# Kernel optimization log

Measured on AMD Instinct MI355X. Metric: run time of the kernel, lower is better.

## Reference

```python
import jax, jax.numpy as jnp
import numpy as np

P = 2          # SamplesLoss p=2
BLUR = 0.05    # eps_final = BLUR**P = 0.0025
SCALING = 0.8  # annealing factor per iteration (on the blur scale)


def _cost(x, y):
    # geomloss cost for p=2: |x - y|^2 / 2, shape (N, M)
    x2 = jnp.sum(x * x, axis=-1)
    y2 = jnp.sum(y * y, axis=-1)
    return 0.5 * (x2[:, None] + y2[None, :] - 2.0 * (x @ y.T))


def _softmin(eps, C, h):
    # -eps * log sum_j exp(h_j - C_ij / eps); h already contains log-weights
    return -eps * jax.nn.logsumexp(h[None, :] - C / eps, axis=1)


def _eps_schedule(x, y):
    # geomloss scaling_parameters / epsilon_schedule with diameter from bounding box
    xn, yn = np.asarray(x), np.asarray(y)
    mins = np.minimum(xn.min(0), yn.min(0))
    maxs = np.maximum(xn.max(0), yn.max(0))
    diameter = float(np.linalg.norm(maxs - mins))
    eps_list = ([diameter ** P]
                + [float(np.exp(e)) for e in np.arange(P * np.log(diameter), P * np.log(BLUR), P * np.log(SCALING))]
                + [BLUR ** P])
    return eps_list


def _sinkhorn_divergence(x, y, eps_list):
    # Debiased Sinkhorn divergence S_eps(x, y), geomloss sinkhorn_tensorized
    N, M = x.shape[0], y.shape[0]
    sg = jax.lax.stop_gradient
    C_xy, C_yx = _cost(x, y), _cost(y, x)
    C_xx, C_yy = _cost(x, sg(x)), _cost(y, sg(y))  # geomloss detaches 2nd arg
    # The annealing loop runs with autograd disabled in geomloss:
    Cxy_, Cyx_, Cxx_, Cyy_ = sg(C_xy), sg(C_yx), sg(C_xx), sg(C_yy)
    a_log = jnp.full((N,), -np.log(N), dtype=x.dtype)  # log uniform weights
    b_log = jnp.full((M,), -np.log(M), dtype=y.dtype)
    e0 = eps_list[0]
    f_aa = _softmin(e0, Cxx_, a_log)
    g_bb = _softmin(e0, Cyy_, b_log)
    g_ab = _softmin(e0, Cyx_, a_log)
    f_ba = _softmin(e0, Cxy_, b_log)
    for eps in eps_list:  # fixed schedule, not a data-dim loop
        ft_ba = _softmin(eps, Cxy_, b_log + g_ab / eps)
        gt_ab = _softmin(eps, Cyx_, a_log + f_ba / eps)
        ft_aa = _softmin(eps, Cxx_, a_log + f_aa / eps)
        gt_bb = _softmin(eps, Cyy_, b_log + g_bb / eps)
        f_ba, g_ab = 0.5 * (f_ba + ft_ba), 0.5 * (g_ab + gt_ab)
        f_aa, g_bb = 0.5 * (f_aa + ft_aa), 0.5 * (g_bb + gt_bb)
    # Final extrapolation step (the only one geomloss differentiates through):
    eps = eps_list[-1]
    f_ba, g_ab = (_softmin(eps, C_xy, sg(b_log + g_ab / eps)),
                  _softmin(eps, C_yx, sg(a_log + f_ba / eps)))
    f_aa = _softmin(eps, C_xx, sg(a_log + f_aa / eps))
    g_bb = _softmin(eps, C_yy, sg(b_log + g_bb / eps))
    # scal with uniform weights == mean
    return jnp.mean(f_ba - f_aa) + jnp.mean(g_ab - g_bb)


def setup_inputs() -> dict:
    key = jax.random.key(0)
    kx, kt = jax.random.split(key)
    x = jax.random.normal(kx, (4096, 64), dtype=jnp.float32)
    target = jax.random.normal(kt, (4096, 64), dtype=jnp.float32)
    return {"x": x, "target": target}


def reference(x, target):
    eps_list = _eps_schedule(x, target)  # concrete schedule from data diameter
    return _sinkhorn_divergence(x, target, eps_list)
```

## Files before the change

### kernel.cpp

```cpp
#include <hip/hip_runtime.h>
#include <math.h>

#define NPTS 4096
#define DIM  64
#define MAX_ITERS 37

#define ALOG (-8.317766166719343f)
#define L2E  (1.4426950408889634f)
#define LN2  (0.6931471805599453f)

#if __has_builtin(__builtin_amdgcn_exp2f)
#define EXP2F(x) __builtin_amdgcn_exp2f(x)
#else
#define EXP2F(x) exp2f(x)
#endif
#if __has_builtin(__builtin_amdgcn_logf)
#define LOG2F(x) __builtin_amdgcn_logf(x)
#else
#define LOG2F(x) log2f(x)
#endif

typedef _Float16 f16x8 __attribute__((ext_vector_type(8)));
typedef float    f32x4 __attribute__((ext_vector_type(4)));

__device__ __forceinline__ void multi_barrier(int* st, int idx, int nsub,
                                              int* lsense) {
    __syncthreads();
    if (threadIdx.x == 0) {
        int s = *lsense ^ 1;
        __threadfence();
        int sub = idx >> 5;
        int prev = __hip_atomic_fetch_add(st + sub * 16, 1, __ATOMIC_ACQ_REL,
                                          __HIP_MEMORY_SCOPE_AGENT);
        if (prev == 31) {
            int pm = __hip_atomic_fetch_add(st + 512, 1, __ATOMIC_ACQ_REL,
                                            __HIP_MEMORY_SCOPE_AGENT);
            if (pm == nsub - 1) {
                for (int i = 0; i < nsub; i++)
                    __hip_atomic_store(st + i * 16, 0, __ATOMIC_RELAXED,
                                       __HIP_MEMORY_SCOPE_AGENT);
                __hip_atomic_store(st + 512, 0, __ATOMIC_RELAXED,
                                   __HIP_MEMORY_SCOPE_AGENT);
                __hip_atomic_store(st + 544, s, __ATOMIC_RELEASE,
                                   __HIP_MEMORY_SCOPE_AGENT);
            } else {
                while (__hip_atomic_load(st + 544, __ATOMIC_ACQUIRE,
                                         __HIP_MEMORY_SCOPE_AGENT) != s)
                    __builtin_amdgcn_s_sleep(8);
            }
        } else {
            while (__hip_atomic_load(st + 544, __ATOMIC_ACQUIRE,
                                     __HIP_MEMORY_SCOPE_AGENT) != s)
                __builtin_amdgcn_s_sleep(8);
        }
        *lsense = s;
        __threadfence();
    }
    __syncthreads();
}

__device__ __forceinline__ void multi_barrier_g(int* st, int idx, int nsub,
                                                int* lsense) {
    __syncthreads();
    if (threadIdx.x == 0) {
        int s = *lsense ^ 1;
        __threadfence();
        int sub = idx >> 5;
        int prev = __hip_atomic_fetch_add(st + sub * 16, 1, __ATOMIC_ACQ_REL,
                                          __HIP_MEMORY_SCOPE_AGENT);
        if (prev == 31) {
            int pm = __hip_atomic_fetch_add(st + 1536, 1, __ATOMIC_ACQ_REL,
                                            __HIP_MEMORY_SCOPE_AGENT);
            if (pm == nsub - 1) {
                for (int i = 0; i < nsub; i++)
                    __hip_atomic_store(st + i * 16, 0, __ATOMIC_RELAXED,
                                       __HIP_MEMORY_SCOPE_AGENT);
                __hip_atomic_store(st + 1536, 0, __ATOMIC_RELAXED,
                                   __HIP_MEMORY_SCOPE_AGENT);
                __hip_atomic_store(st + 1600, s, __ATOMIC_RELEASE,
                                   __HIP_MEMORY_SCOPE_AGENT);
            } else {
                while (__hip_atomic_load(st + 1600, __ATOMIC_ACQUIRE,
                                         __HIP_MEMORY_SCOPE_AGENT) != s)
                    __builtin_amdgcn_s_sleep(8);
            }
        } else {
            while (__hip_atomic_load(st + 1600, __ATOMIC_ACQUIRE,
                                     __HIP_MEMORY_SCOPE_AGENT) != s)
                __builtin_amdgcn_s_sleep(8);
        }
        *lsense = s;
        __threadfence();
    }
    __syncthreads();
}

__global__ __launch_bounds__(256, 8) void mega8_kernel(
        const float* __restrict__ x, const float* __restrict__ y,
        _Float16* __restrict__ X16, _Float16* __restrict__ Y16,
        float* __restrict__ x2, float* __restrict__ y2,
        float* __restrict__ pmn, float* __restrict__ pmx,
        int* hdr, float* __restrict__ sched,
        float* __restrict__ F, float* __restrict__ H, float* __restrict__ P,
        int* bar, float* __restrict__ out)
{
    const int b  = blockIdx.x;
    const int tt = threadIdx.x;
    int senseG = 0, senseL = 0;

    int* stL = bar + (b >> 10) * 2048;
    int* stG = bar + 2 * 2048;
    const int idxL = b & 1023;

    __shared__ float hs[256];
    __shared__ _Float16 Bs[2][64][72];

    {
        int g = b * 256 + tt;
        if (g < NPTS * DIM) {
            float xv = x[g], yv = y[g];
            X16[g] = (_Float16)xv;
            Y16[g] = (_Float16)yv;
            float sx = xv * xv, sy = yv * yv;
            for (int o = 32; o > 0; o >>= 1) {
                sx += __shfl_xor(sx, o, 64);
                sy += __shfl_xor(sy, o, 64);
            }
            if ((tt & 63) == 0) { x2[g >> 6] = sx; y2[g >> 6] = sy; }
        }
        if (b < 128) {
            float mn = INFINITY, mx = -INFINITY;
            for (int gg = b * 256 + tt; gg < NPTS * DIM; gg += 128 * 256) {
                float v = x[gg]; mn = fminf(mn, v); mx = fmaxf(mx, v);
                float w = y[gg]; mn = fminf(mn, w); mx = fmaxf(mx, w);
            }
            float* smn = hs;
            float* smx = (float*)&Bs[0][0][0];
            smn[tt] = mn; smx[tt] = mx;
            __syncthreads();
            if (tt < 64) {
                for (int qq = 1; qq < 4; qq++) {
                    mn = fminf(mn, smn[tt + 64 * qq]);
                    mx = fmaxf(mx, smx[tt + 64 * qq]);
                }
                pmn[b * 64 + tt] = mn;
                pmx[b * 64 + tt] = mx;
            }
        }
    }
    multi_barrier_g(stG, b, 64, &senseG);

    if (b == 0) {
        float* r2 = hs;
        if (tt < 64) {
            float mn = INFINITY, mx = -INFINITY;
            for (int bb = 0; bb < 128; bb++) {
                mn = fminf(mn, pmn[bb * 64 + tt]);
                mx = fmaxf(mx, pmx[bb * 64 + tt]);
            }
            float range = mx - mn;
            r2[tt] = range * range;
        }
        __syncthreads();
        if (tt == 0) {
            float ss = 0.f;
            for (int k = 0; k < 64; k++) ss += r2[k];
            float diam_f = sqrtf(ss);
            double diam = (double)diam_f;
            double start = 2.0 * log(diam);
            double stop  = 2.0 * log(0.05);
            double step  = 2.0 * log(0.8);
            int n_ar = (int)ceil((stop - start) / step);
            if (n_ar < 0) n_ar = 0;
            int ne = n_ar + 2;
            if (ne > 63) ne = 63;
            sched[0] = (float)(diam * diam);
            for (int k = 0; k < n_ar && (1 + k) < 63; k++)
                sched[1 + k] = (float)exp(start + step * (double)k);
            sched[ne - 1] = 0.0025f;
            for (int k = ne; k < 64; k++) sched[k] = 0.0025f;
            hdr[0] = ne;
        }
    }
    multi_barrier_g(stG, b, 64, &senseG);

    const int n_eps = *(volatile int*)hdr;

    const int mat = b >> 9, rb = (b >> 4) & 31, cs = b & 15;
    const _Float16* Am = (mat == 0 || mat == 2) ? X16 : Y16;
    const _Float16* Bm = (mat == 1 || mat == 2) ? X16 : Y16;
    const int matc = (mat < 2) ? (1 - mat) : mat;
    const float* sqc = (matc == 0 || matc == 2) ? x2 : y2;
    const int c0 = cs * 256, r0 = rb * 128;
    const int wv = tt >> 6, lane = tt & 63, q = lane >> 4, lo = lane & 15;
    const int srow = tt >> 2, scol = (tt & 3) * 16;

    f16x8 a[2][2];
#pragma unroll
    for (int rt = 0; rt < 2; rt++) {
        const _Float16* ar = Am + (size_t)(r0 + wv * 32 + rt * 16 + lo) * DIM + q * 8;
        a[rt][0] = *(const f16x8*)ar;
        a[rt][1] = *(const f16x8*)(ar + 32);
    }
    const _Float16* Bsrc0 = Bm + (size_t)(c0 + srow) * DIM + scol;

    for (int p = 0; p <= n_eps + 2; p++) {
        const int t = (p == 0) ? -2 : (p == n_eps + 2) ? -1 : (p - 1);
        const bool do_main = (t < 0) || (t < n_eps);

        f16x8 t0a, t0b;
        if (do_main) {
            t0a = *(const f16x8*)Bsrc0;
            t0b = *(const f16x8*)(Bsrc0 + 8);
        }

        if (t == -2) {
            float inv2i = L2E / sched[0];
            hs[tt] = ALOG * L2E - 0.5f * sqc[c0 + tt] * inv2i;
        } else if (t == -1) {
            hs[tt] = H[mat * 4096 + c0 + tt];
        } else {
            int pp = (t == 0) ? 1 : ((t - 1) & 1);
            const float* Pm = P + pp * 524288;
            const float* Ps = Pm + 262144;
            float epsp = sched[(t == 0) ? 0 : (t - 1)];
            float inv2c = L2E / sched[t];
            int row = c0 + tt;
            int base = (matc * 16) * NPTS + row;
            float M = -INFINITY;
#pragma unroll
            for (int qq = 0; qq < 16; qq++) M = fmaxf(M, Pm[base + qq * NPTS]);
            float S = 0.f;
#pragma unroll
            for (int qq = 0; qq < 16; qq++)
                S += Ps[base + qq * NPTS] * EXP2F(Pm[base + qq * NPTS] - M);
            float sq = sqc[row];
            float res = 0.5f * sq - epsp * LN2 * (M + LOG2F(S));
            float fnew = (t == 0) ? res
                       : 0.5f * (F[((t - 1) & 1) * 16384 + matc * 4096 + row] + res);
            float h = ALOG * L2E + (fnew - 0.5f * sq) * inv2c;
            hs[tt] = h;
            if (rb == 0) {
                F[(t & 1) * 16384 + matc * 4096 + row] = fnew;
                H[mat * 4096 + row] = h;
            }
        }

        if (do_main) {
            int idx = (t == -2) ? 0 : ((t == -1) ? n_eps - 1 : t);
            float inv2 = L2E / sched[idx];

            *(f16x8*)&Bs[0][srow][scol]     = t0a;
            *(f16x8*)&Bs[0][srow][scol + 8] = t0b;

            float m[2] = { -INFINITY, -INFINITY };
            float s[2] = { 0.f, 0.f };

            for (int ct = 0; ct < 4; ct++) {
                __syncthreads();
                f16x8 n0, n1;
                if (ct < 3) {
                    const _Float16* src = Bsrc0 + (size_t)(ct + 1) * 64 * DIM;
                    n0 = *(const f16x8*)src;
                    n1 = *(const f16x8*)(src + 8);
                }
                const _Float16 (*Bt)[72] = Bs[ct & 1];
#pragma unroll
                for (int cc = 0; cc < 4; cc++) {
                    const _Float16* br = &Bt[cc * 16 + lo][q * 8];
                    f16x8 b0 = *(const f16x8*)br;
                    f16x8 b1 = *(const f16x8*)(br + 32);
                    f32x4 hv = *(const f32x4*)&hs[ct * 64 + cc * 16 + q * 4];
#pragma unroll
                    for (int rt = 0; rt < 2; rt++) {
                        f32x4 acc = {0.f, 0.f, 0.f, 0.f};
                        acc = __builtin_amdgcn_mfma_f32_16x16x32_f16(b0, a[rt][0], acc, 0, 0, 0);
                        acc = __builtin_amdgcn_mfma_f32_16x16x32_f16(b1, a[rt][1], acc, 0, 0, 0);
                        float v0 = fmaf(acc[0], inv2, hv[0]);
                        float v1 = fmaf(acc[1], inv2, hv[1]);
                        float v2 = fmaf(acc[2], inv2, hv[2]);
                        float v3 = fmaf(acc[3], inv2, hv[3]);
                        float lm = fmaxf(fmaxf(v0, v1), fmaxf(v2, v3));
                        if (__any(lm > m[rt] + 40.0f)) {
                            float nm = fmaxf(m[rt], lm);
                            s[rt] *= EXP2F(m[rt] - nm);
                            m[rt] = nm;
                        }
                        if (lm > m[rt] - 26.0f) {
                            float mm = m[rt];
                            s[rt] += (EXP2F(v0 - mm) + EXP2F(v1 - mm))
                                   + (EXP2F(v2 - mm) + EXP2F(v3 - mm));
                        }
                    }
                }
                if (ct < 3) {
                    *(f16x8*)&Bs[(ct + 1) & 1][srow][scol]     = n0;
                    *(f16x8*)&Bs[(ct + 1) & 1][srow][scol + 8] = n1;
                }
            }

            float ml[2] = { m[0], m[1] };
#pragma unroll
            for (int off = 16; off < 64; off <<= 1)
#pragma unroll
                for (int rt = 0; rt < 2; rt++)
                    m[rt] = fmaxf(m[rt], __shfl_xor(m[rt], off, 64));
#pragma unroll
            for (int rt = 0; rt < 2; rt++)
                s[rt] *= EXP2F(ml[rt] - m[rt]);
#pragma unroll
            for (int off = 16; off < 64; off <<= 1)
#pragma unroll
                for (int rt = 0; rt < 2; rt++)
                    s[rt] += __shfl_xor(s[rt], off, 64);

            if (q == 0) {
                int pw = (t == -1) ? (n_eps & 1) : ((t == -2) ? 1 : (t & 1));
                float* Pw = P + pw * 524288;
                float* Sw = Pw + 262144;
#pragma unroll
                for (int rt = 0; rt < 2; rt++) {
                    int row = r0 + wv * 32 + rt * 16 + lo;
                    Pw[(mat * 16 + cs) * NPTS + row] = m[rt];
                    Sw[(mat * 16 + cs) * NPTS + row] = s[rt];
                }
            }
        }
        multi_barrier_g(stL, idxL, 32, &senseL);
    }

    multi_barrier_g(stG, b, 64, &senseG);

    if (b < 64) {
        const float* Pm = P + (n_eps & 1) * 524288;
        const float* Ps = Pm + 262144;
        int g = b * 256 + tt;
        int fmat = g >> 12, row = g & 4095;
        float eps = sched[n_eps - 1];
        const float* sqr = (fmat == 0 || fmat == 2) ? x2 : y2;
        int base = (fmat * 16) * NPTS + row;
        float M = -INFINITY;
#pragma unroll
        for (int qq = 0; qq < 16; qq++) M = fmaxf(M, Pm[base + qq * NPTS]);
        float S = 0.f;
#pragma unroll
        for (int qq = 0; qq < 16; qq++)
            S += Ps[base + qq * NPTS] * EXP2F(Pm[base + qq * NPTS] - M);
        float res = 0.5f * sqr[row] - eps * LN2 * (M + LOG2F(S));
        float val = ((fmat < 2) ? res : -res) * (1.0f / NPTS);
        float* sh = hs;
        sh[tt] = val;
        __syncthreads();
        for (int o = 128; o > 0; o >>= 1) {
            if (tt < o) sh[tt] += sh[tt + o];
            __syncthreads();
        }
        if (tt == 0) atomicAdd(out, sh[0]);
    }
}

template <int TPB>
__global__ __launch_bounds__(256, (TPB == 1 ? 4 : 2)) void mega_kernel(
        const float* __restrict__ x, const float* __restrict__ y,
        _Float16* __restrict__ X16, _Float16* __restrict__ Y16,
        float* __restrict__ x2, float* __restrict__ y2,
        float* __restrict__ pmn, float* __restrict__ pmx,
        int* hdr, float* __restrict__ sched,
        float* __restrict__ F, float* __restrict__ H, float* __restrict__ P,
        int* bar, float* __restrict__ out)
{
    const int b  = blockIdx.x;
    const int tt = threadIdx.x;
    int senseG = 0, senseL = 0;

    int* stG;  int nsubG;
    int* stL;  int idxL; int nsubL;
    if (TPB == 1) {
        stG = bar + 2048; nsubG = 32;
        stL = bar + (b >> 9) * 1024; idxL = b & 511; nsubL = 16;
    } else {
        stG = bar + 2048; nsubG = 16;
        stL = stG; idxL = b; nsubL = 16;
    }
    int* senseLp = (TPB == 1) ? &senseL : &senseG;

    __shared__ float hs[512];
    __shared__ _Float16 Bs[2][64][72];

    for (int g = b * 256 + tt; g < NPTS * DIM; g += gridDim.x * 256) {
        float xv = x[g], yv = y[g];
        X16[g] = (_Float16)xv;
        Y16[g] = (_Float16)yv;
        float sx = xv * xv, sy = yv * yv;
        for (int o = 32; o > 0; o >>= 1) {
            sx += __shfl_xor(sx, o, 64);
            sy += __shfl_xor(sy, o, 64);
        }
        if ((tt & 63) == 0) { x2[g >> 6] = sx; y2[g >> 6] = sy; }
    }
    if (b < 128) {
        float mn = INFINITY, mx = -INFINITY;
        for (int gg = b * 256 + tt; gg < NPTS * DIM; gg += 128 * 256) {
            float v = x[gg]; mn = fminf(mn, v); mx = fmaxf(mx, v);
            float w = y[gg]; mn = fminf(mn, w); mx = fmaxf(mx, w);
        }
        float* smn = hs;
        float* smx = (float*)&Bs[0][0][0];
        smn[tt] = mn; smx[tt] = mx;
        __syncthreads();
        if (tt < 64) {
            for (int qq = 1; qq < 4; qq++) {
                mn = fminf(mn, smn[tt + 64 * qq]);
                mx = fmaxf(mx, smx[tt + 64 * qq]);
            }
            pmn[b * 64 + tt] = mn;
            pmx[b * 64 + tt] = mx;
        }
    }
    multi_barrier(stG, b, nsubG, &senseG);

    if (b == 0) {
        float* r2 = hs;
        if (tt < 64) {
            float mn = INFINITY, mx = -INFINITY;
            for (int bb = 0; bb < 128; bb++) {
                mn = fminf(mn, pmn[bb * 64 + tt]);
                mx = fmaxf(mx, pmx[bb * 64 + tt]);
            }
            float range = mx - mn;
            r2[tt] = range * range;
        }
        __syncthreads();
        if (tt == 0) {
            float ss = 0.f;
            for (int k = 0; k < 64; k++) ss += r2[k];
            float diam_f = sqrtf(ss);
            double diam = (double)diam_f;
            double start = 2.0 * log(diam);
            double stop  = 2.0 * log(0.05);
            double step  = 2.0 * log(0.8);
            int n_ar = (int)ceil((stop - start) / step);
            if (n_ar < 0) n_ar = 0;
            int ne = n_ar + 2;
            if (ne > 63) ne = 63;
            sched[0] = (float)(diam * diam);
            for (int k = 0; k < n_ar && (1 + k) < 63; k++)
                sched[1 + k] = (float)exp(start + step * (double)k);
            sched[ne - 1] = 0.0025f;
            for (int k = ne; k < 64; k++) sched[k] = 0.0025f;
            hdr[0] = ne;
        }
    }
    multi_barrier(stG, b, nsubG, &senseG);

    const int n_eps = *(volatile int*)hdr;

    const int wv = tt >> 6, lane = tt & 63, q = lane >> 4, lo = lane & 15;
    const int srow = tt >> 2, scol = (tt & 3) * 16;

    f16x8 a[TPB][2][2];
#pragma unroll
    for (int sub = 0; sub < TPB; sub++) {
        const int bt = b + 512 * sub;
        const int mat_ = bt >> 8, rb_ = (bt >> 3) & 31;
        const _Float16* Am = (mat_ == 0 || mat_ == 2) ? X16 : Y16;
        const int r0_ = rb_ * 128;
#pragma unroll
        for (int rt = 0; rt < 2; rt++) {
            const _Float16* ar = Am + (size_t)(r0_ + wv * 32 + rt * 16 + lo) * DIM + q * 8;
            a[sub][rt][0] = *(const f16x8*)ar;
            a[sub][rt][1] = *(const f16x8*)(ar + 32);
        }
    }

    for (int p = 0; p <= n_eps + 2; p++) {
        const int t = (p == 0) ? -2 : (p == n_eps + 2) ? -1 : (p - 1);
        const bool do_main = (t < 0) || (t < n_eps);

#pragma unroll
        for (int sub = 0; sub < TPB; sub++) {
            const int bt = b + 512 * sub;
            const int mat = bt >> 8, rb = (bt >> 3) & 31, cs = bt & 7;
            const _Float16* Bm = (mat == 1 || mat == 2) ? X16 : Y16;
            const int matc = (mat < 2) ? (1 - mat) : mat;
            const float* sqc = (matc == 0 || matc == 2) ? x2 : y2;
            const int c0 = cs * 512, r0 = rb * 128;
            const _Float16* Bsrc0 = Bm + (size_t)(c0 + srow) * DIM + scol;

            f16x8 t0a, t0b;
            if (do_main) {
                t0a = *(const f16x8*)Bsrc0;
                t0b = *(const f16x8*)(Bsrc0 + 8);
            }

            if (t == -2) {
                float inv2i = L2E / sched[0];
                for (int r = tt; r < 512; r += 256)
                    hs[r] = ALOG * L2E - 0.5f * sqc[c0 + r] * inv2i;
            } else if (t == -1) {
                for (int r = tt; r < 512; r += 256)
                    hs[r] = H[mat * 4096 + c0 + r];
            } else {
                int pp = (t == 0) ? 1 : ((t - 1) & 1);
                const float* Pm = P + pp * 262144;
                const float* Ps = Pm + 131072;
                float epsp = sched[(t == 0) ? 0 : (t - 1)];
                float inv2c = L2E / sched[t];
                for (int r = tt; r < 512; r += 256) {
                    int row = c0 + r;
                    int base = (matc * 8) * NPTS + row;
                    float M = -INFINITY;
#pragma unroll
                    for (int qq = 0; qq < 8; qq++) M = fmaxf(M, Pm[base + qq * NPTS]);
// ... 291 lines not shown
    float inv2 = L2E / sched[idx];

    int wv = tt >> 6, lane = tt & 63, q = lane >> 4, lo = lane & 15;

    f16x8 a[2][2];
#pragma unroll
    for (int rt = 0; rt < 2; rt++) {
        const _Float16* ar = Am + (size_t)(r0 + wv * 32 + rt * 16 + lo) * DIM + q * 8;
        a[rt][0] = *(const f16x8*)ar;
        a[rt][1] = *(const f16x8*)(ar + 32);
    }

    int srow = tt >> 2, scol = (tt & 3) * 16;
    {
        const _Float16* src = Bm + (size_t)(c0 + srow) * DIM + scol;
        *(f16x8*)&Bs[0][srow][scol]     = *(const f16x8*)src;
        *(f16x8*)&Bs[0][srow][scol + 8] = *(const f16x8*)(src + 8);
    }

    float m[2][4], s[2][4];
#pragma unroll
    for (int rt = 0; rt < 2; rt++)
#pragma unroll
        for (int r = 0; r < 4; r++) { m[rt][r] = -INFINITY; s[rt][r] = 0.f; }

    for (int ct = 0; ct < 8; ct++) {
        __syncthreads();
        f16x8 n0, n1;
        if (ct < 7) {
            const _Float16* src = Bm + (size_t)(c0 + (ct + 1) * 64 + srow) * DIM + scol;
            n0 = *(const f16x8*)src;
            n1 = *(const f16x8*)(src + 8);
        }
        const _Float16 (*Bt)[72] = Bs[ct & 1];
        float v[2][4][4];
#pragma unroll
        for (int cc = 0; cc < 4; cc++) {
            const _Float16* br = &Bt[cc * 16 + lo][q * 8];
            f16x8 b0 = *(const f16x8*)br;
            f16x8 b1 = *(const f16x8*)(br + 32);
            float hval = hs[ct * 64 + cc * 16 + lo];
#pragma unroll
            for (int rt = 0; rt < 2; rt++) {
                f32x4 acc = {0.f, 0.f, 0.f, 0.f};
                acc = __builtin_amdgcn_mfma_f32_16x16x32_f16(a[rt][0], b0, acc, 0, 0, 0);
                acc = __builtin_amdgcn_mfma_f32_16x16x32_f16(a[rt][1], b1, acc, 0, 0, 0);
#pragma unroll
                for (int r = 0; r < 4; r++) v[rt][r][cc] = fmaf(acc[r], inv2, hval);
            }
        }
#pragma unroll
        for (int rt = 0; rt < 2; rt++)
#pragma unroll
            for (int r = 0; r < 4; r++) {
                float lm = fmaxf(fmaxf(v[rt][r][0], v[rt][r][1]),
                                 fmaxf(v[rt][r][2], v[rt][r][3]));
                if (lm > m[rt][r] - 26.0f) {
                    float nm = fmaxf(m[rt][r], lm);
                    float acc = s[rt][r] * EXP2F(m[rt][r] - nm);
                    acc += EXP2F(v[rt][r][0] - nm) + EXP2F(v[rt][r][1] - nm)
                         + EXP2F(v[rt][r][2] - nm) + EXP2F(v[rt][r][3] - nm);
                    m[rt][r] = nm; s[rt][r] = acc;
                }
            }
        if (ct < 7) {
            *(f16x8*)&Bs[(ct + 1) & 1][srow][scol]     = n0;
            *(f16x8*)&Bs[(ct + 1) & 1][srow][scol + 8] = n1;
        }
    }

#pragma unroll
    for (int off = 1; off < 16; off <<= 1) {
#pragma unroll
        for (int rt = 0; rt < 2; rt++)
#pragma unroll
            for (int r = 0; r < 4; r++) {
                float om = __shfl_xor(m[rt][r], off, 64);
                float os = __shfl_xor(s[rt][r], off, 64);
                float nm = fmaxf(m[rt][r], om);
                s[rt][r] = s[rt][r] * EXP2F(m[rt][r] - nm) + os * EXP2F(om - nm);
                m[rt][r] = nm;
            }
    }
    if (lo == 0) {
        int pw = (t == -1) ? (n_eps & 1) : ((t == -2) ? 1 : (t & 1));
        float* Pm = P + pw * 262144;
        float* Ps = Pm + 131072;
#pragma unroll
        for (int rt = 0; rt < 2; rt++)
#pragma unroll
            for (int r = 0; r < 4; r++) {
                int row = r0 + wv * 32 + rt * 16 + q * 4 + r;
                Pm[(mat * 8 + cs) * NPTS + row] = m[rt][r];
                Ps[(mat * 8 + cs) * NPTS + row] = s[rt][r];
            }
    }
}

__global__ void finalize_kernel(const float* __restrict__ P,
                                const float* __restrict__ x2, const float* __restrict__ y2,
                                const int* __restrict__ hdr, const float* __restrict__ sched,
                                float* __restrict__ out) {
    int n_eps = hdr[0];
    const float* Pm = P + (n_eps & 1) * 262144;
    const float* Ps = Pm + 131072;
    int g = blockIdx.x * 256 + threadIdx.x;
    int mat = g >> 12, row = g & 4095;
    float eps = sched[n_eps - 1];
    const float* sqr = (mat == 0 || mat == 2) ? x2 : y2;
    int base = (mat * 8) * NPTS + row;
    float M = -INFINITY;
#pragma unroll
    for (int q = 0; q < 8; q++) M = fmaxf(M, Pm[base + q * NPTS]);
    float S = 0.f;
#pragma unroll
    for (int q = 0; q < 8; q++) S += Ps[base + q * NPTS] * EXP2F(Pm[base + q * NPTS] - M);
    float res = 0.5f * sqr[row] - eps * LN2 * (M + LOG2F(S));
    float val = ((mat == 0 || mat == 1) ? res : -res) * (1.0f / NPTS);
    __shared__ float sh[256];
    sh[threadIdx.x] = val;
    __syncthreads();
    for (int o = 128; o > 0; o >>= 1) {
        if (threadIdx.x < o) sh[threadIdx.x] += sh[threadIdx.x + o];
        __syncthreads();
    }
    if (threadIdx.x == 0) atomicAdd(out, sh[0]);
}

extern "C" void kernel_launch(void* const* d_in, const int* in_sizes, int n_in,
                              void* d_out, int out_size, void* d_ws, size_t ws_size,
                              hipStream_t stream) {
    const float* x = (const float*)d_in[0];
    const float* y = (const float*)d_in[1];
    float* out = (float*)d_out;
    float* w = (float*)d_ws;

    int*   hdr   = (int*)w;
    float* sched = w + 16;
    float* pmn   = w + 80;
    float* pmx   = w + 8272;
    float* x2    = w + 16464;
    float* y2    = w + 20560;
    float* F     = w + 24656;
    float* H     = w + 57424;
    float* P     = w + 73808;

    _Float16* X16c = (_Float16*)(w + 598096);
    _Float16* Y16c = (_Float16*)(w + 729168);
    int*      barc = (int*)(w + 860240);

    _Float16* X16e = (_Float16*)(w + 1122384);
    _Float16* Y16e = (_Float16*)(w + 1253456);
    int*      bare = (int*)(w + 1384528);
    const size_t ws_need_e = (size_t)(1384528 + 6144 + 64) * 4;

    hipMemsetAsync(out, 0, sizeof(float), stream);

    int occ8 = 0, occ1 = 0, occ2 = 0;
    (void)hipOccupancyMaxActiveBlocksPerMultiprocessor(&occ8, mega8_kernel, 256, 0);
    (void)hipOccupancyMaxActiveBlocksPerMultiprocessor(&occ1, mega_kernel<1>, 256, 0);
    (void)hipOccupancyMaxActiveBlocksPerMultiprocessor(&occ2, mega_kernel<2>, 256, 0);

    if (occ8 >= 8 && ws_size >= ws_need_e) {
        hipMemsetAsync(bare, 0, 3 * 2048 * sizeof(int), stream);
        hipLaunchKernelGGL(mega8_kernel, dim3(2048), dim3(256), 0, stream,
                           x, y, X16e, Y16e, x2, y2, pmn, pmx, hdr, sched,
                           F, H, P, bare, out);
    } else if (occ1 >= 4) {
        hipMemsetAsync(barc, 0, 3 * 1024 * sizeof(int), stream);
        hipLaunchKernelGGL((mega_kernel<1>), dim3(1024), dim3(256), 0, stream,
                           x, y, X16c, Y16c, x2, y2, pmn, pmx, hdr, sched,
                           F, H, P, barc, out);
    } else if (occ2 >= 2) {
        hipMemsetAsync(barc, 0, 3 * 1024 * sizeof(int), stream);
        hipLaunchKernelGGL((mega_kernel<2>), dim3(512), dim3(256), 0, stream,
                           x, y, X16c, Y16c, x2, y2, pmn, pmx, hdr, sched,
                           F, H, P, barc, out);
    } else {
        hipLaunchKernelGGL(minmax_part_kernel, dim3(128), dim3(256), 0, stream, x, y, pmn, pmx);
        hipLaunchKernelGGL(schedule_kernel, dim3(1), dim3(64), 0, stream, pmn, pmx, hdr, sched);
        hipLaunchKernelGGL(sqnorm_kernel, dim3(1024), dim3(256), 0, stream, x, x2);
        hipLaunchKernelGGL(sqnorm_kernel, dim3(1024), dim3(256), 0, stream, y, y2);
        hipLaunchKernelGGL(cast_kernel, dim3(1024), dim3(256), 0, stream, x, y, X16c, Y16c);
        hipLaunchKernelGGL(pass_kernel, dim3(1024), dim3(256), 0, stream,
                           X16c, Y16c, x2, y2, F, H, P, hdr, sched, -2);
        for (int t = 0; t < MAX_ITERS; t++)
            hipLaunchKernelGGL(pass_kernel, dim3(1024), dim3(256), 0, stream,
                               X16c, Y16c, x2, y2, F, H, P, hdr, sched, t);
        hipLaunchKernelGGL(pass_kernel, dim3(1024), dim3(256), 0, stream,
                           X16c, Y16c, x2, y2, F, H, P, hdr, sched, -1);
        hipLaunchKernelGGL(finalize_kernel, dim3(64), dim3(256), 0, stream,
                           P, x2, y2, hdr, sched, out);
    }
}
```

Before: 959.4 us.

## Split per-iteration combine into few dedicated blocks with two fence-free barriers

```diff
diff --git a/kernel.cpp b/kernel.cpp
--- a/kernel.cpp
+++ b/kernel.cpp
@@ -22,6 +22,320 @@
 
 typedef _Float16 f16x8 __attribute__((ext_vector_type(8)));
 typedef float    f32x4 __attribute__((ext_vector_type(4)));
+
+__device__ __forceinline__ float aload(const float* p) {
+    return __hip_atomic_load(p, __ATOMIC_RELAXED, __HIP_MEMORY_SCOPE_AGENT);
+}
+__device__ __forceinline__ void astore(float* p, float v) {
+    __hip_atomic_store(p, v, __ATOMIC_RELAXED, __HIP_MEMORY_SCOPE_AGENT);
+}
+
+template <bool FENCE>
+__device__ __forceinline__ void gbar(int* st, int idx, int nsub, int* lsense) {
+    __syncthreads();
+    if (threadIdx.x == 0) {
+        int s = *lsense ^ 1;
+        if (FENCE) __threadfence();
+        int sub = idx >> 5;
+        int prev = __hip_atomic_fetch_add(st + sub * 16, 1, __ATOMIC_ACQ_REL,
+                                          __HIP_MEMORY_SCOPE_AGENT);
+        if (prev == 31) {
+            int pm = __hip_atomic_fetch_add(st + 1536, 1, __ATOMIC_ACQ_REL,
+                                            __HIP_MEMORY_SCOPE_AGENT);
+            if (pm == nsub - 1) {
+                for (int i = 0; i < nsub; i++)
+                    __hip_atomic_store(st + i * 16, 0, __ATOMIC_RELAXED,
+                                       __HIP_MEMORY_SCOPE_AGENT);
+                __hip_atomic_store(st + 1536, 0, __ATOMIC_RELAXED,
+                                   __HIP_MEMORY_SCOPE_AGENT);
+                __hip_atomic_store(st + 1600, s, __ATOMIC_RELEASE,
+                                   __HIP_MEMORY_SCOPE_AGENT);
+            } else {
+                while (__hip_atomic_load(st + 1600, __ATOMIC_ACQUIRE,
+                                         __HIP_MEMORY_SCOPE_AGENT) != s)
+                    __builtin_amdgcn_s_sleep(8);
+            }
+        } else {
+            while (__hip_atomic_load(st + 1600, __ATOMIC_ACQUIRE,
+                                     __HIP_MEMORY_SCOPE_AGENT) != s)
+                __builtin_amdgcn_s_sleep(8);
+        }
+        *lsense = s;
+        if (FENCE) __threadfence();
+    }
+    __syncthreads();
+}
+
+__global__ __launch_bounds__(256, 8) void mega9_kernel(
+        const float* __restrict__ x, const float* __restrict__ y,
+        _Float16* __restrict__ X16, _Float16* __restrict__ Y16,
+        float* __restrict__ x2, float* __restrict__ y2,
+        float* __restrict__ pmn, float* __restrict__ pmx,
+        int* hdr, float* __restrict__ sched,
+        float* H, float* P,
+        int* bar, float* __restrict__ out)
+{
+    const int b  = blockIdx.x;
+    const int tt = threadIdx.x;
+    int senseA = 0, senseB = 0, senseG = 0;
+
+    const int grp = b >> 10;
+    int* barA = bar + grp * 2048;
+    int* barB = bar + 4096 + grp * 2048;
+    int* barG = bar + 8192;
+    const int idxL = b & 1023;
+
+    __shared__ float hs[256];
+    __shared__ _Float16 Bs[2][64][72];
+
+    {
+        int g = b * 256 + tt;
+        if (g < NPTS * DIM) {
+            float xv = x[g], yv = y[g];
+            X16[g] = (_Float16)xv;
+            Y16[g] = (_Float16)yv;
+            float sx = xv * xv, sy = yv * yv;
+            for (int o = 32; o > 0; o >>= 1) {
+                sx += __shfl_xor(sx, o, 64);
+                sy += __shfl_xor(sy, o, 64);
+            }
+            if ((tt & 63) == 0) { x2[g >> 6] = sx; y2[g >> 6] = sy; }
+        }
+        if (b < 128) {
+            float mn = INFINITY, mx = -INFINITY;
+            for (int gg = b * 256 + tt; gg < NPTS * DIM; gg += 128 * 256) {
+                float v = x[gg]; mn = fminf(mn, v); mx = fmaxf(mx, v);
+                float w = y[gg]; mn = fminf(mn, w); mx = fmaxf(mx, w);
+            }
+            float* smn = hs;
+            float* smx = (float*)&Bs[0][0][0];
+            smn[tt] = mn; smx[tt] = mx;
+            __syncthreads();
+            if (tt < 64) {
+                for (int qq = 1; qq < 4; qq++) {
+                    mn = fminf(mn, smn[tt + 64 * qq]);
+                    mx = fmaxf(mx, smx[tt + 64 * qq]);
+                }
+                pmn[b * 64 + tt] = mn;
+                pmx[b * 64 + tt] = mx;
+            }
+        }
+    }
+    gbar<true>(barG, b, 64, &senseG);
+
+    if (b == 0) {
+        float* r2 = hs;
+        if (tt < 64) {
+            float mn = INFINITY, mx = -INFINITY;
+            for (int bb = 0; bb < 128; bb++) {
+                mn = fminf(mn, pmn[bb * 64 + tt]);
+                mx = fmaxf(mx, pmx[bb * 64 + tt]);
+            }
+            float range = mx - mn;
+            r2[tt] = range * range;
+        }
+        __syncthreads();
+        if (tt == 0) {
+            float ss = 0.f;
+            for (int k = 0; k < 64; k++) ss += r2[k];
+            float diam_f = sqrtf(ss);
+            double diam = (double)diam_f;
+            double start = 2.0 * log(diam);
+            double stop  = 2.0 * log(0.05);
+            double step  = 2.0 * log(0.8);
+            int n_ar = (int)ceil((stop - start) / step);
+            if (n_ar < 0) n_ar = 0;
+            int ne = n_ar + 2;
+            if (ne > 63) ne = 63;
+            sched[0] = (float)(diam * diam);
+            for (int k = 0; k < n_ar && (1 + k) < 63; k++)
+                sched[1 + k] = (float)exp(start + step * (double)k);
+            sched[ne - 1] = 0.0025f;
+            for (int k = ne; k < 64; k++) sched[k] = 0.0025f;
+            hdr[0] = ne;
+        }
+    }
+    gbar<true>(barG, b, 64, &senseG);
+
+    const int n_eps = *(volatile int*)hdr;
+
+    const int mat = b >> 9, rb = (b >> 4) & 31, cs = b & 15;
+    const _Float16* Am = (mat == 0 || mat == 2) ? X16 : Y16;
+    const _Float16* Bm = (mat == 1 || mat == 2) ? X16 : Y16;
+    const int matc = (mat < 2) ? (1 - mat) : mat;
+    const float* sqc = (matc == 0 || matc == 2) ? x2 : y2;
+    const int c0 = cs * 256, r0 = rb * 128;
+    const int wv = tt >> 6, lane = tt & 63, q = lane >> 4, lo = lane & 15;
+    const int srow = tt >> 2, scol = (tt & 3) * 16;
+
+    f16x8 a[2][2];
+#pragma unroll
+    for (int rt = 0; rt < 2; rt++) {
+        const _Float16* ar = Am + (size_t)(r0 + wv * 32 + rt * 16 + lo) * DIM + q * 8;
+        a[rt][0] = *(const f16x8*)ar;
+        a[rt][1] = *(const f16x8*)(ar + 32);
+    }
+    const _Float16* Bsrc0 = Bm + (size_t)(c0 + srow) * DIM + scol;
+
+    const bool isComb = (rb < 4) && (tt < 64);
+    int   combRow = 0;
+    float combSq = 0.f, fprev = 0.f;
+    if (rb < 4) {
+        combRow = (cs * 4 + rb) * 64 + (tt & 63);
+        combSq  = sqc[combRow];
+    }
+
+    auto run_main = [&](int t) {
+        f16x8 t0a = *(const f16x8*)Bsrc0;
+        f16x8 t0b = *(const f16x8*)(Bsrc0 + 8);
+
+        if (t == -2) {
+            float inv2i = L2E / sched[0];
+            hs[tt] = ALOG * L2E - 0.5f * sqc[c0 + tt] * inv2i;
+        } else {
+            hs[tt] = aload(&H[mat * 4096 + c0 + tt]);
+        }
+
+        int idx = (t == -2) ? 0 : ((t == -1) ? n_eps - 1 : t);
+        float inv2 = L2E / sched[idx];
+
+        *(f16x8*)&Bs[0][srow][scol]     = t0a;
+        *(f16x8*)&Bs[0][srow][scol + 8] = t0b;
+
+        float m[2] = { -INFINITY, -INFINITY };
+        float s[2] = { 0.f, 0.f };
+
+        for (int ct = 0; ct < 4; ct++) {
+            __syncthreads();
+            f16x8 n0, n1;
+            if (ct < 3) {
+                const _Float16* src = Bsrc0 + (size_t)(ct + 1) * 64 * DIM;
+                n0 = *(const f16x8*)src;
+                n1 = *(const f16x8*)(src + 8);
+            }
+            const _Float16 (*Bt)[72] = Bs[ct & 1];
+#pragma unroll
+            for (int cc = 0; cc < 4; cc++) {
+                const _Float16* br = &Bt[cc * 16 + lo][q * 8];
+                f16x8 b0 = *(const f16x8*)br;
+                f16x8 b1 = *(const f16x8*)(br + 32);
+                f32x4 hv = *(const f32x4*)&hs[ct * 64 + cc * 16 + q * 4];
+#pragma unroll
+                for (int rt = 0; rt < 2; rt++) {
+                    f32x4 acc = {0.f, 0.f, 0.f, 0.f};
+                    acc = __builtin_amdgcn_mfma_f32_16x16x32_f16(b0, a[rt][0], acc, 0, 0, 0);
+                    acc = __builtin_amdgcn_mfma_f32_16x16x32_f16(b1, a[rt][1], acc, 0, 0, 0);
+                    float v0 = fmaf(acc[0], inv2, hv[0]);
+                    float v1 = fmaf(acc[1], inv2, hv[1]);
+                    float v2 = fmaf(acc[2], inv2, hv[2]);
+                    float v3 = fmaf(acc[3], inv2, hv[3]);
+                    float lm = fmaxf(fmaxf(v0, v1), fmaxf(v2, v3));
+                    if (__any(lm > m[rt] + 40.0f)) {
+                        float nm = fmaxf(m[rt], lm);
+                        s[rt] *= EXP2F(m[rt] - nm);
+                        m[rt] = nm;
+                    }
+                    if (lm > m[rt] - 26.0f) {
+                        float mm = m[rt];
+                        s[rt] += (EXP2F(v0 - mm) + EXP2F(v1 - mm))
+                               + (EXP2F(v2 - mm) + EXP2F(v3 - mm));
+                    }
+                }
+            }
+            if (ct < 3) {
+                *(f16x8*)&Bs[(ct + 1) & 1][srow][scol]     = n0;
+                *(f16x8*)&Bs[(ct + 1) & 1][srow][scol + 8] = n1;
+            }
+        }
+
+        float ml[2] = { m[0], m[1] };
+#pragma unroll
+        for (int off = 16; off < 64; off <<= 1)
+#pragma unroll
+            for (int rt = 0; rt < 2; rt++)
+                m[rt] = fmaxf(m[rt], __shfl_xor(m[rt], off, 64));
+#pragma unroll
+        for (int rt = 0; rt < 2; rt++)
+            s[rt] *= EXP2F(ml[rt] - m[rt]);
+#pragma unroll
+        for (int off = 16; off < 64; off <<= 1)
+#pragma unroll
+            for (int rt = 0; rt < 2; rt++)
+                s[rt] += __shfl_xor(s[rt], off, 64);
+
+        if (q == 0) {
+            int pw = (t == -1) ? (n_eps & 1) : ((t == -2) ? 1 : (t & 1));
+            float* Pw = P + pw * 524288;
+            float* Sw = Pw + 262144;
+#pragma unroll
+            for (int rt = 0; rt < 2; rt++) {
+                int row = r0 + wv * 32 + rt * 16 + lo;
+                astore(&Pw[(mat * 16 + cs) * NPTS + row], m[rt]);
+                astore(&Sw[(mat * 16 + cs) * NPTS + row], s[rt]);
+            }
+        }
+        __syncthreads();
+    };
+
+    run_main(-2);
+    for (int c = 0; c <= n_eps; c++) {
+        gbar<false>(barA, idxL, 32, &senseA);
+        if (isComb) {
+            int pp = (c == 0) ? 1 : ((c - 1) & 1);
+            const float* Pm = P + pp * 524288;
+            const float* Ps = Pm + 262144;
+            float epsp  = sched[(c == 0) ? 0 : (c - 1)];
+            float inv2c = L2E / sched[c];
+            int base = (matc * 16) * NPTS + combRow;
+            float M = -INFINITY, S = 0.f;
+#pragma unroll
+            for (int qq = 0; qq < 16; qq++) {
+                float pv = aload(&Pm[base + qq * NPTS]);
+                float sv = aload(&Ps[base + qq * NPTS]);
+                if (pv > M) { S *= EXP2F(M - pv); M = pv; }
+                S += sv * EXP2F(pv - M);
+            }
+            float res  = 0.5f * combSq - epsp * LN2 * (M + LOG2F(S));
+            float fnew = (c == 0) ? res : 0.5f * (fprev + res);
+            fprev = fnew;
+            astore(&H[mat * 4096 + combRow],
+                   ALOG * L2E + (fnew - 0.5f * combSq) * inv2c);
+        }
+        gbar<false>(barB, idxL, 32, &senseB);
+        if (c < n_eps) run_main(c);
+    }
+    run_main(-1);
+
+    gbar<true>(barG, b, 64, &senseG);
+
+    if (b < 64) {
+        const float* Pm = P + (n_eps & 1) * 524288;
+        const float* Ps = Pm + 262144;
+        int g = b * 256 + tt;
+        int fmat = g >> 12, row = g & 4095;
+        float eps = sched[n_eps - 1];
+        const float* sqr = (fmat == 0 || fmat == 2) ? x2 : y2;
+        int base = (fmat * 16) * NPTS + row;
+        float M = -INFINITY, S = 0.f;
+#pragma unroll
+        for (int qq = 0; qq < 16; qq++) {
+            float pv = aload(&Pm[base + qq * NPTS]);
+            float sv = aload(&Ps[base + qq * NPTS]);
+            if (pv > M) { S *= EXP2F(M - pv); M = pv; }
+            S += sv * EXP2F(pv - M);
+        }
+        float res = 0.5f * sqr[row] - eps * LN2 * (M + LOG2F(S));
+        float val = ((fmat < 2) ? res : -res) * (1.0f / NPTS);
+        float* sh = hs;
+        sh[tt] = val;
+        __syncthreads();
+        for (int o = 128; o > 0; o >>= 1) {
+            if (tt < o) sh[tt] += sh[tt + o];
+            __syncthreads();
+        }
+        if (tt == 0) atomicAdd(out, sh[0]);
+    }
+}
 
 __device__ __forceinline__ void multi_barrier(int* st, int idx, int nsub,
                                               int* lsense) {
@@ -59,306 +373,6 @@
     __syncthreads();
 }
 
-__device__ __forceinline__ void multi_barrier_g(int* st, int idx, int nsub,
-                                                int* lsense) {
-    __syncthreads();
-    if (threadIdx.x == 0) {
-        int s = *lsense ^ 1;
-        __threadfence();
-        int sub = idx >> 5;
-        int prev = __hip_atomic_fetch_add(st + sub * 16, 1, __ATOMIC_ACQ_REL,
-                                          __HIP_MEMORY_SCOPE_AGENT);
-        if (prev == 31) {
-            int pm = __hip_atomic_fetch_add(st + 1536, 1, __ATOMIC_ACQ_REL,
-                                            __HIP_MEMORY_SCOPE_AGENT);
-            if (pm == nsub - 1) {
-                for (int i = 0; i < nsub; i++)
-                    __hip_atomic_store(st + i * 16, 0, __ATOMIC_RELAXED,
-                                       __HIP_MEMORY_SCOPE_AGENT);
-                __hip_atomic_store(st + 1536, 0, __ATOMIC_RELAXED,
-                                   __HIP_MEMORY_SCOPE_AGENT);
-                __hip_atomic_store(st + 1600, s, __ATOMIC_RELEASE,
-                                   __HIP_MEMORY_SCOPE_AGENT);
-            } else {
-                while (__hip_atomic_load(st + 1600, __ATOMIC_ACQUIRE,
-                                         __HIP_MEMORY_SCOPE_AGENT) != s)
-                    __builtin_amdgcn_s_sleep(8);
-            }
-        } else {
-            while (__hip_atomic_load(st + 1600, __ATOMIC_ACQUIRE,
-                                     __HIP_MEMORY_SCOPE_AGENT) != s)
-                __builtin_amdgcn_s_sleep(8);
-        }
-        *lsense = s;
-        __threadfence();
-    }
-    __syncthreads();
-}
-
-__global__ __launch_bounds__(256, 8) void mega8_kernel(
-        const float* __restrict__ x, const float* __restrict__ y,
-        _Float16* __restrict__ X16, _Float16* __restrict__ Y16,
-        float* __restrict__ x2, float* __restrict__ y2,
-        float* __restrict__ pmn, float* __restrict__ pmx,
-        int* hdr, float* __restrict__ sched,
-        float* __restrict__ F, float* __restrict__ H, float* __restrict__ P,
-        int* bar, float* __restrict__ out)
-{
-    const int b  = blockIdx.x;
-    const int tt = threadIdx.x;
-    int senseG = 0, senseL = 0;
-
-    int* stL = bar + (b >> 10) * 2048;
-    int* stG = bar + 2 * 2048;
-    const int idxL = b & 1023;
-
-    __shared__ float hs[256];
-    __shared__ _Float16 Bs[2][64][72];
-
-    {
-        int g = b * 256 + tt;
-        if (g < NPTS * DIM) {
-            float xv = x[g], yv = y[g];
-            X16[g] = (_Float16)xv;
-            Y16[g] = (_Float16)yv;
-            float sx = xv * xv, sy = yv * yv;
-            for (int o = 32; o > 0; o >>= 1) {
-                sx += __shfl_xor(sx, o, 64);
-                sy += __shfl_xor(sy, o, 64);
-            }
-            if ((tt & 63) == 0) { x2[g >> 6] = sx; y2[g >> 6] = sy; }
-        }
-        if (b < 128) {
-            float mn = INFINITY, mx = -INFINITY;
-            for (int gg = b * 256 + tt; gg < NPTS * DIM; gg += 128 * 256) {
-                float v = x[gg]; mn = fminf(mn, v); mx = fmaxf(mx, v);
-                float w = y[gg]; mn = fminf(mn, w); mx = fmaxf(mx, w);
-            }
-            float* smn = hs;
-            float* smx = (float*)&Bs[0][0][0];
-            smn[tt] = mn; smx[tt] = mx;
-            __syncthreads();
-            if (tt < 64) {
-                for (int qq = 1; qq < 4; qq++) {
-                    mn = fminf(mn, smn[tt + 64 * qq]);
-                    mx = fmaxf(mx, smx[tt + 64 * qq]);
-                }
-                pmn[b * 64 + tt] = mn;
-                pmx[b * 64 + tt] = mx;
-            }
-        }
-    }
-    multi_barrier_g(stG, b, 64, &senseG);
-
-    if (b == 0) {
-        float* r2 = hs;
-        if (tt < 64) {
-            float mn = INFINITY, mx = -INFINITY;
-            for (int bb = 0; bb < 128; bb++) {
-                mn = fminf(mn, pmn[bb * 64 + tt]);
-                mx = fmaxf(mx, pmx[bb * 64 + tt]);
-            }
-            float range = mx - mn;
-            r2[tt] = range * range;
-        }
-        __syncthreads();
-        if (tt == 0) {
-            float ss = 0.f;
-            for (int k = 0; k < 64; k++) ss += r2[k];
-            float diam_f = sqrtf(ss);
-            double diam = (double)diam_f;
-            double start = 2.0 * log(diam);
-            double stop  = 2.0 * log(0.05);
-            double step  = 2.0 * log(0.8);
-            int n_ar = (int)ceil((stop - start) / step);
-            if (n_ar < 0) n_ar = 0;
-            int ne = n_ar + 2;
-            if (ne > 63) ne = 63;
-            sched[0] = (float)(diam * diam);
-            for (int k = 0; k < n_ar && (1 + k) < 63; k++)
-                sched[1 + k] = (float)exp(start + step * (double)k);
-            sched[ne - 1] = 0.0025f;
-            for (int k = ne; k < 64; k++) sched[k] = 0.0025f;
-            hdr[0] = ne;
-        }
-    }
-    multi_barrier_g(stG, b, 64, &senseG);
-
-    const int n_eps = *(volatile int*)hdr;
-
-    const int mat = b >> 9, rb = (b >> 4) & 31, cs = b & 15;
-    const _Float16* Am = (mat == 0 || mat == 2) ? X16 : Y16;
-    const _Float16* Bm = (mat == 1 || mat == 2) ? X16 : Y16;
-    const int matc = (mat < 2) ? (1 - mat) : mat;
-    const float* sqc = (matc == 0 || matc == 2) ? x2 : y2;
-    const int c0 = cs * 256, r0 = rb * 128;
-    const int wv = tt >> 6, lane = tt & 63, q = lane >> 4, lo = lane & 15;
-    const int srow = tt >> 2, scol = (tt & 3) * 16;
-
-    f16x8 a[2][2];
-#pragma unroll
-    for (int rt = 0; rt < 2; rt++) {
-        const _Float16* ar = Am + (size_t)(r0 + wv * 32 + rt * 16 + lo) * DIM + q * 8;
-        a[rt][0] = *(const f16x8*)ar;
-        a[rt][1] = *(const f16x8*)(ar + 32);
-    }
-    const _Float16* Bsrc0 = Bm + (size_t)(c0 + srow) * DIM + scol;
-
-    for (int p = 0; p <= n_eps + 2; p++) {
-        const int t = (p == 0) ? -2 : (p == n_eps + 2) ? -1 : (p - 1);
-        const bool do_main = (t < 0) || (t < n_eps);
-
-        f16x8 t0a, t0b;
-        if (do_main) {
-            t0a = *(const f16x8*)Bsrc0;
-            t0b = *(const f16x8*)(Bsrc0 + 8);
-        }
-
-        if (t == -2) {
-            float inv2i = L2E / sched[0];
-            hs[tt] = ALOG * L2E - 0.5f * sqc[c0 + tt] * inv2i;
-        } else if (t == -1) {
-            hs[tt] = H[mat * 4096 + c0 + tt];
-        } else {
-            int pp = (t == 0) ? 1 : ((t - 1) & 1);
-            const float* Pm = P + pp * 524288;
-            const float* Ps = Pm + 262144;
-            float epsp = sched[(t == 0) ? 0 : (t - 1)];
-            float inv2c = L2E / sched[t];
-            int row = c0 + tt;
-            int base = (matc * 16) * NPTS + row;
-            float M = -INFINITY;
-#pragma unroll
-            for (int qq = 0; qq < 16; qq++) M = fmaxf(M, Pm[base + qq * NPTS]);
-            float S = 0.f;
-#pragma unroll
-            for (int qq = 0; qq < 16; qq++)
-                S += Ps[base + qq * NPTS] * EXP2F(Pm[base + qq * NPTS] - M);
-            float sq = sqc[row];
-            float res = 0.5f * sq - epsp * LN2 * (M + LOG2F(S));
-            float fnew = (t == 0) ? res
-                       : 0.5f * (F[((t - 1) & 1) * 16384 + matc * 4096 + row] + res);
-            float h = ALOG * L2E + (fnew - 0.5f * sq) * inv2c;
-            hs[tt] = h;
-            if (rb == 0) {
-                F[(t & 1) * 16384 + matc * 4096 + row] = fnew;
-                H[mat * 4096 + row] = h;
-            }
-        }
-
-        if (do_main) {
-            int idx = (t == -2) ? 0 : ((t == -1) ? n_eps - 1 : t);
-            float inv2 = L2E / sched[idx];
-
-            *(f16x8*)&Bs[0][srow][scol]     = t0a;
-            *(f16x8*)&Bs[0][srow][scol + 8] = t0b;
-
-            float m[2] = { -INFINITY, -INFINITY };
-            float s[2] = { 0.f, 0.f };
-
-            for (int ct = 0; ct < 4; ct++) {
-                __syncthreads();
-                f16x8 n0, n1;
-                if (ct < 3) {
-                    const _Float16* src = Bsrc0 + (size_t)(ct + 1) * 64 * DIM;
-                    n0 = *(const f16x8*)src;
-                    n1 = *(const f16x8*)(src + 8);
-                }
-                const _Float16 (*Bt)[72] = Bs[ct & 1];
-#pragma unroll
-                for (int cc = 0; cc < 4; cc++) {
-                    const _Float16* br = &Bt[cc * 16 + lo][q * 8];
-                    f16x8 b0 = *(const f16x8*)br;
-                    f16x8 b1 = *(const f16x8*)(br + 32);
-                    f32x4 hv = *(const f32x4*)&hs[ct * 64 + cc * 16 + q * 4];
-#pragma unroll
-                    for (int rt = 0; rt < 2; rt++) {
-                        f32x4 acc = {0.f, 0.f, 0.f, 0.f};
-                        acc = __builtin_amdgcn_mfma_f32_16x16x32_f16(b0, a[rt][0], acc, 0, 0, 0);
-                        acc = __builtin_amdgcn_mfma_f32_16x16x32_f16(b1, a[rt][1], acc, 0, 0, 0);
-                        float v0 = fmaf(acc[0], inv2, hv[0]);
-                        float v1 = fmaf(acc[1], inv2, hv[1]);
-                        float v2 = fmaf(acc[2], inv2, hv[2]);
-                        float v3 = fmaf(acc[3], inv2, hv[3]);
-                        float lm = fmaxf(fmaxf(v0, v1), fmaxf(v2, v3));
-                        if (__any(lm > m[rt] + 40.0f)) {
-                            float nm = fmaxf(m[rt], lm);
-                            s[rt] *= EXP2F(m[rt] - nm);
-                            m[rt] = nm;
-                        }
-                        if (lm > m[rt] - 26.0f) {
-                            float mm = m[rt];
-                            s[rt] += (EXP2F(v0 - mm) + EXP2F(v1 - mm))
-                                   + (EXP2F(v2 - mm) + EXP2F(v3 - mm));
-                        }
-                    }
-                }
-                if (ct < 3) {
-                    *(f16x8*)&Bs[(ct + 1) & 1][srow][scol]     = n0;
-                    *(f16x8*)&Bs[(ct + 1) & 1][srow][scol + 8] = n1;
-                }
-            }
-
-            float ml[2] = { m[0], m[1] };
-#pragma unroll
-            for (int off = 16; off < 64; off <<= 1)
-#pragma unroll
-                for (int rt = 0; rt < 2; rt++)
-                    m[rt] = fmaxf(m[rt], __shfl_xor(m[rt], off, 64));
-#pragma unroll
-            for (int rt = 0; rt < 2; rt++)
-                s[rt] *= EXP2F(ml[rt] - m[rt]);
-#pragma unroll
-            for (int off = 16; off < 64; off <<= 1)
-#pragma unroll
-                for (int rt = 0; rt < 2; rt++)
-                    s[rt] += __shfl_xor(s[rt], off, 64);
-
-            if (q == 0) {
-                int pw = (t == -1) ? (n_eps & 1) : ((t == -2) ? 1 : (t & 1));
-                float* Pw = P + pw * 524288;
-                float* Sw = Pw + 262144;
-#pragma unroll
-                for (int rt = 0; rt < 2; rt++) {
-                    int row = r0 + wv * 32 + rt * 16 + lo;
-                    Pw[(mat * 16 + cs) * NPTS + row] = m[rt];
-                    Sw[(mat * 16 + cs) * NPTS + row] = s[rt];
-                }
-            }
-        }
-        multi_barrier_g(stL, idxL, 32, &senseL);
-    }
-
-    multi_barrier_g(stG, b, 64, &senseG);
-
-    if (b < 64) {
-        const float* Pm = P + (n_eps & 1) * 524288;
-        const float* Ps = Pm + 262144;
-        int g = b * 256 + tt;
-        int fmat = g >> 12, row = g & 4095;
-        float eps = sched[n_eps - 1];
-        const float* sqr = (fmat == 0 || fmat == 2) ? x2 : y2;
-        int base = (fmat * 16) * NPTS + row;
-        float M = -INFINITY;
-#pragma unroll
-        for (int qq = 0; qq < 16; qq++) M = fmaxf(M, Pm[base + qq * NPTS]);
-        float S = 0.f;
-#pragma unroll
-        for (int qq = 0; qq < 16; qq++)
-            S += Ps[base + qq * NPTS] * EXP2F(Pm[base + qq * NPTS] - M);
-        float res = 0.5f * sqr[row] - eps * LN2 * (M + LOG2F(S));
-        float val = ((fmat < 2) ? res : -res) * (1.0f / NPTS);
-        float* sh = hs;
-        sh[tt] = val;
-        __syncthreads();
-        for (int o = 128; o > 0; o >>= 1) {
-            if (tt < o) sh[tt] += sh[tt + o];
-            __syncthreads();
-        }
-        if (tt == 0) atomicAdd(out, sh[0]);
-    }
-}
-
 template <int TPB>
 __global__ __launch_bounds__(256, (TPB == 1 ? 4 : 2)) void mega_kernel(
         const float* __restrict__ x, const float* __restrict__ y,
@@ -956,20 +970,20 @@
     _Float16* X16e = (_Float16*)(w + 1122384);
     _Float16* Y16e = (_Float16*)(w + 1253456);
     int*      bare = (int*)(w + 1384528);
-    const size_t ws_need_e = (size_t)(1384528 + 6144 + 64) * 4;
+    const size_t ws_need_e = (size_t)(1384528 + 10240 + 16) * 4;
 
     hipMemsetAsync(out, 0, sizeof(float), stream);
 
-    int occ8 = 0, occ1 = 0, occ2 = 0;
-    (void)hipOccupancyMaxActiveBlocksPerMultiprocessor(&occ8, mega8_kernel, 256, 0);
+    int occ9 = 0, occ1 = 0, occ2 = 0;
+    (void)hipOccupancyMaxActiveBlocksPerMultiprocessor(&occ9, mega9_kernel, 256, 0);
     (void)hipOccupancyMaxActiveBlocksPerMultiprocessor(&occ1, mega_kernel<1>, 256, 0);
     (void)hipOccupancyMaxActiveBlocksPerMultiprocessor(&occ2, mega_kernel<2>, 256, 0);
 
-    if (occ8 >= 8 && ws_size >= ws_need_e) {
-        hipMemsetAsync(bare, 0, 3 * 2048 * sizeof(int), stream);
-        hipLaunchKernelGGL(mega8_kernel, dim3(2048), dim3(256), 0, stream,
+    if (occ9 >= 8 && ws_size >= ws_need_e) {
+        hipMemsetAsync(bare, 0, 5 * 2048 * sizeof(int), stream);
+        hipLaunchKernelGGL(mega9_kernel, dim3(2048), dim3(256), 0, stream,
                            x, y, X16e, Y16e, x2, y2, pmn, pmx, hdr, sched,
-                           F, H, P, bare, out);
+                           H, P, bare, out);
     } else if (occ1 >= 4) {
         hipMemsetAsync(barc, 0, 3 * 1024 * sizeof(int), stream);
         hipLaunchKernelGGL((mega_kernel<1>), dim3(1024), dim3(256), 0, stream,
```

New measurement: 981.8 us. 2.3% more time.
